# Performance work log

Measured on AMD Instinct MI355X. Metric: run time of the kernel, lower is better.

The kernel has to match this reference:

```python
import jax, jax.numpy as jnp
import numpy as np

NUM_NODES = 100000
NUM_EDGES = 1600000
FEAT = 128
HID = 128
NUM_GRAPHS = 512


def setup_inputs() -> dict:
    key = jax.random.key(0)
    ks = jax.random.split(key, 8)
    x = jax.random.normal(ks[0], (NUM_NODES, FEAT), dtype=jnp.float32)
    edge_index = jax.random.randint(ks[1], (2, NUM_EDGES), 0, NUM_NODES, dtype=jnp.int64)
    batch = jnp.sort(jax.random.randint(ks[2], (NUM_NODES,), 0, NUM_GRAPHS, dtype=jnp.int64))
    # Glorot-ish init for weights (scale named for clarity)
    s1 = 1.0 / np.sqrt(FEAT)
    s2 = 1.0 / np.sqrt(HID)
    W1 = jax.random.normal(ks[3], (FEAT, HID), dtype=jnp.float32) * s1
    b1 = jnp.zeros((HID,), dtype=jnp.float32)
    W2 = jax.random.normal(ks[4], (HID, HID), dtype=jnp.float32) * s2
    b2 = jnp.zeros((HID,), dtype=jnp.float32)
    Wout = jax.random.normal(ks[5], (HID, 1), dtype=jnp.float32) * s2
    bout = jnp.zeros((1,), dtype=jnp.float32)
    return {"x": x, "edge_index": edge_index, "batch": batch,
            "W1": W1, "b1": b1, "W2": W2, "b2": b2, "Wout": Wout, "bout": bout}


def reference(x, edge_index, batch, W1, b1, W2, b2, Wout, bout):
    N = x.shape[0]
    # PyG GCNConv: add self-loops, symmetric normalization D^-1/2 (A+I) D^-1/2
    loops = jnp.arange(N, dtype=edge_index.dtype)
    src = jnp.concatenate([edge_index[0], loops])  # [E+N]
    dst = jnp.concatenate([edge_index[1], loops])  # [E+N]
    ones = jnp.ones_like(dst, dtype=x.dtype)
    deg = jax.ops.segment_sum(ones, dst, num_segments=N)  # in-degree incl. self-loop
    dinv = jnp.where(deg > 0, jax.lax.rsqrt(deg), 0.0)
    coeff = (dinv[src] * dinv[dst])[:, None]  # [E+N, 1]

    def gcn(h, W, b):
        h = h @ W                                       # [N, H] dense GEMM
        msg = h[src] * coeff                            # gather + scale
        agg = jax.ops.segment_sum(msg, dst, num_segments=N)  # scatter-add
        return agg + b

    h = jax.nn.relu(gcn(x, W1, b1))
    h = jax.nn.relu(gcn(h, W2, b2))

    # global_mean_pool over batch ids
    G = NUM_GRAPHS
    sums = jax.ops.segment_sum(h, batch, num_segments=G)
    cnts = jax.ops.segment_sum(jnp.ones((N,), dtype=h.dtype), batch, num_segments=G)
    pooled = sums / jnp.maximum(cnts, 1.0)[:, None]

    return pooled @ Wout + bout  # [G, 1]
```

## Files before the change

### kernel.cpp

```cpp
#include <hip/hip_runtime.h>
#include <hip/hip_bf16.h>
#include <hip/hip_fp16.h>

#define FEAT 128
#define PSLOTS 64
#define BCAP 5120
#define NBIN 512

typedef _Float16 h8 __attribute__((ext_vector_type(8)));
typedef float f4 __attribute__((ext_vector_type(4)));
typedef float fx2 __attribute__((ext_vector_type(2)));


__device__ __forceinline__ void wt_body(const float* __restrict__ W1,
                                        const float* __restrict__ W2,
                                        __half* __restrict__ Wt1,
                                        __half* __restrict__ Wt2, int bid) {
    int t = bid * 256 + threadIdx.x;
    const float* W = (t < 8192) ? W1 : W2;
    __half* Wt     = (t < 8192) ? Wt1 : Wt2;
    int u = t & 8191;
    int n = u >> 6, k2 = (u & 63) * 2;
    float a = W[(size_t)k2 * 128 + n];
    float b = W[(size_t)(k2 + 1) * 128 + n];
    ((__half2*)Wt)[n * 64 + (k2 >> 1)] = __floats2half2_rn(a, b);
}

__device__ __forceinline__ void bin_body(const int* __restrict__ ei, int E, int chunk,
                                         int* __restrict__ cursor,
                                         unsigned* __restrict__ binned, int nb,
                                         int bid, int* smem) {
    int* hist = smem;
    int* base = smem + 512;
    int start = bid * chunk;
    int end = start + chunk; if (end > E) end = E;
    for (int i = threadIdx.x; i < nb; i += 256) hist[i] = 0;
    __syncthreads();
    for (int e = start + threadIdx.x; e < end; e += 256)
        atomicAdd(&hist[ei[E + e] >> 8], 1);
    __syncthreads();
    for (int i = threadIdx.x; i < nb; i += 256) {
        int h = hist[i];
        base[i] = h ? atomicAdd(&cursor[i], h) : 0;
    }
    __syncthreads();
    for (int e = start + threadIdx.x; e < end; e += 256) {
        int s = ei[e];
        int d = ei[E + e];
        int b = d >> 8;
        int pos = atomicAdd(&base[b], 1);
        if (pos < BCAP)
            binned[(size_t)b * BCAP + pos] = (unsigned)s | ((unsigned)(d & 255) << 17);
    }
}

__global__ __launch_bounds__(256) void bin_wt(const int* __restrict__ ei, int E, int chunk,
                                              int* __restrict__ cursor,
                                              unsigned* __restrict__ binned, int nb,
                                              const float* __restrict__ W1,
                                              const float* __restrict__ W2,
                                              __half* __restrict__ Wt1,
                                              __half* __restrict__ Wt2) {
    __shared__ int smem[1024];
    if ((int)blockIdx.x < NBIN)
        bin_body(ei, E, chunk, cursor, binned, nb, blockIdx.x, smem);
    else
        wt_body(W1, W2, Wt1, Wt2, blockIdx.x - NBIN);
}


__device__ __forceinline__ void loadA(const __half* p, int quad, h8* a) {
#pragma unroll
    for (int ks = 0; ks < 4; ++ks)
        a[ks] = *(const h8*)(p + ks * 32 + quad * 8);
}
__device__ __forceinline__ void loadA(const float* p, int quad, h8* a) {
#pragma unroll
    for (int ks = 0; ks < 4; ++ks) {
        const float* q = p + ks * 32 + quad * 8;
        float4 f0 = *(const float4*)q;
        float4 f1 = *(const float4*)(q + 4);
        h8 v;
        v[0] = (_Float16)f0.x; v[1] = (_Float16)f0.y;
        v[2] = (_Float16)f0.z; v[3] = (_Float16)f0.w;
        v[4] = (_Float16)f1.x; v[5] = (_Float16)f1.y;
        v[6] = (_Float16)f1.z; v[7] = (_Float16)f1.w;
        a[ks] = v;
    }
}

template <typename TIN>
__device__ __forceinline__ void gemm_body(const TIN* __restrict__ X,
                                          const __half* __restrict__ Wt,
                                          unsigned char* __restrict__ Y, int N,
                                          const int* __restrict__ deg,
                                          int bid, _Float16* Bs) {
    {
        const float4* src = (const float4*)Wt;
        float4* dst = (float4*)Bs;
        for (int i = threadIdx.x; i < 2048; i += 256) {
            int n = i >> 4, ch = i & 15;
            dst[n * 16 + (ch ^ (n & 15))] = src[i];
        }
    }
    __syncthreads();

    int lane = threadIdx.x & 63;
    int wave = threadIdx.x >> 6;
    int m = lane & 15;
    int quad = lane >> 4;
    int rowb = bid * 128 + wave * 16;

    h8 a[2][4];
#pragma unroll
    for (int rt = 0; rt < 2; ++rt) {
        int rA = rowb + rt * 64 + m; if (rA >= N) rA = N - 1;
        loadA(X + (size_t)rA * FEAT, quad, a[rt]);
    }

    f4 acc[2][8];
#pragma unroll
    for (int rt = 0; rt < 2; ++rt)
#pragma unroll
        for (int nt = 0; nt < 8; ++nt) acc[rt][nt] = (f4){0.f, 0.f, 0.f, 0.f};

#pragma unroll
    for (int nt = 0; nt < 8; ++nt) {
        const _Float16* bbase = Bs + (nt * 16 + m) * 128;
#pragma unroll
        for (int ks = 0; ks < 4; ++ks) {
            int ch = (ks * 4 + quad) ^ m;
            h8 bfrag = *(const h8*)(bbase + ch * 8);
            acc[0][nt] = __builtin_amdgcn_mfma_f32_16x16x32_f16(a[0][ks], bfrag, acc[0][nt], 0, 0, 0);
            acc[1][nt] = __builtin_amdgcn_mfma_f32_16x16x32_f16(a[1][ks], bfrag, acc[1][nt], 0, 0, 0);
        }
    }

#pragma unroll
    for (int rt = 0; rt < 2; ++rt)
#pragma unroll
    for (int r = 0; r < 4; ++r) {
        int row = rowb + rt * 64 + quad * 4 + r;
        if (row < N) {
            float sc = rsqrtf((float)deg[row] + 1.0f);
#pragma unroll
            for (int nt = 0; nt < 8; ++nt) {
                float v = sc * acc[rt][nt][r];
                int pk = __builtin_amdgcn_cvt_pk_fp8_f32(v, v, 0, false);
                Y[(size_t)row * FEAT + nt * 16 + m] = (unsigned char)(pk & 0xFF);
            }
        }
    }
}

template <typename TIN>
__global__ __launch_bounds__(256) void gemm_mfma(const TIN* __restrict__ X,
                                                 const __half* __restrict__ Wt,
                                                 unsigned char* __restrict__ Y,
                                                 const int* __restrict__ deg, int N) {
    __shared__ __align__(16) _Float16 Bs[128 * 128];
    gemm_body<TIN>(X, Wt, Y, N, deg, blockIdx.x, Bs);
}


__global__ __launch_bounds__(256) void k_deg_fill(const unsigned* __restrict__ binned,
                                                  const int* __restrict__ cursor,
                                                  int N, int* __restrict__ deg,
                                                  int* __restrict__ rowstart,
                                                  int* __restrict__ meta, int zoff) {
    __shared__ int ld[256];
    __shared__ int sc[256];
    __shared__ int cur[256];
    int b = blockIdx.x;
    int cnt = cursor[b]; if (cnt > BCAP) cnt = BCAP;
    int s = b * BCAP, e = s + cnt;
    ld[threadIdx.x] = 0;
    __syncthreads();
    for (int i = s + threadIdx.x; i < e; i += 256)
        atomicAdd(&ld[binned[i] >> 17], 1);
    __syncthreads();
    int d = ld[threadIdx.x];
    sc[threadIdx.x] = d;
    __syncthreads();
    for (int off = 1; off < 256; off <<= 1) {
        int t = (threadIdx.x >= off) ? sc[threadIdx.x - off] : 0;
        __syncthreads();
        sc[threadIdx.x] += t;
        __syncthreads();
    }
    int rs = s + sc[threadIdx.x] - d;
    cur[threadIdx.x] = rs;
    int v = (b << 8) + threadIdx.x;
    if (v < N) {
        deg[v] = d;
        rowstart[v] = rs;
    }
    __syncthreads();
    for (int i = s + threadIdx.x; i < e; i += 256) {
        unsigned p = binned[i];
        int src = (int)(p & 0x1FFFF);
        int drl = (int)(p >> 17);
        int pos = atomicAdd(&cur[drl], 1);
        meta[pos] = src << 7;
    }
    int t = cnt + threadIdx.x;
    if (threadIdx.x < 64 && t < BCAP + 64) meta[s + t] = zoff;
}


__device__ __forceinline__ void accum8(uint2 u, fx2* acc) {
    acc[0] += __builtin_amdgcn_cvt_pk_f32_fp8((int)u.x, false);
    acc[1] += __builtin_amdgcn_cvt_pk_f32_fp8((int)u.x, true);
    acc[2] += __builtin_amdgcn_cvt_pk_f32_fp8((int)u.y, false);
    acc[3] += __builtin_amdgcn_cvt_pk_f32_fp8((int)u.y, true);
}

template <bool POOL>
__global__ __launch_bounds__(256) void agg_relu(const unsigned char* __restrict__ Y,
                                                const int* __restrict__ rowstart,
                                                const int* __restrict__ degc,
                                                const int* __restrict__ meta,
                                                const float* __restrict__ bias,
                                                __half* __restrict__ H, int N, int zoff,
                                                const float* __restrict__ Wout,
                                                const int* __restrict__ batch,
                                                float* __restrict__ gsum, int G) {
    int wid  = (blockIdx.x * 256 + threadIdx.x) >> 6;
    int lane = threadIdx.x & 63;
    if (wid >= N) return;
    int v = wid;
    int g = lane >> 4;
    int c = lane & 15;
    int cb = c * 8;
    const char* Ycb = (const char*)Y + cb;

    fx2 acc[4];
#pragma unroll
    for (int k = 0; k < 4; ++k) acc[k] = (fx2){0.f, 0.f};

    {
        int so = (g == 0) ? (v << 7) : zoff;
        uint2 u = *(const uint2*)(Ycb + so);
        accum8(u, acc);
    }

    int base = rowstart[v];
    int n = degc[v];
    int g4 = g * 4;
    for (int i0 = 0; i0 < n; i0 += 16) {
        int o[4];
#pragma unroll
        for (int j = 0; j < 4; ++j) {
            int idx = i0 + g4 + j;
            int mj = meta[base + idx];
            o[j] = (idx < n) ? mj : zoff;
        }
        uint2 u[4];
#pragma unroll
        for (int j = 0; j < 4; ++j)
            u[j] = *(const uint2*)(Ycb + o[j]);
#pragma unroll
        for (int j = 0; j < 4; ++j) accum8(u[j], acc);
    }

#pragma unroll
    for (int k = 0; k < 4; ++k) {
        fx2 t;
        t[0] = __shfl_xor(acc[k][0], 16);
        t[1] = __shfl_xor(acc[k][1], 16);
        acc[k] += t;
        t[0] = __shfl_xor(acc[k][0], 32);
        t[1] = __shfl_xor(acc[k][1], 32);
        acc[k] += t;
    }
    float dv = rsqrtf((float)n + 1.0f);

    if (POOL) {
        const float4* bp = (const float4*)(bias + cb);
        float4 b0 = bp[0], b1 = bp[1];
        const float4* wp = (const float4*)(Wout + cb);
        float4 w0 = wp[0], w1 = wp[1];
        float h0 = fmaxf(dv * acc[0][0] + b0.x, 0.f);
        float h1 = fmaxf(dv * acc[0][1] + b0.y, 0.f);
        float h2 = fmaxf(dv * acc[1][0] + b0.z, 0.f);
        float h3 = fmaxf(dv * acc[1][1] + b0.w, 0.f);
        float h4 = fmaxf(dv * acc[2][0] + b1.x, 0.f);
        float h5 = fmaxf(dv * acc[2][1] + b1.y, 0.f);
        float h6 = fmaxf(dv * acc[3][0] + b1.z, 0.f);
        float h7 = fmaxf(dv * acc[3][1] + b1.w, 0.f);
        float s = h0 * w0.x + h1 * w0.y + h2 * w0.z + h3 * w0.w
                + h4 * w1.x + h5 * w1.y + h6 * w1.z + h7 * w1.w;
        if (g == 0) {
            s += __shfl_xor(s, 1);
            s += __shfl_xor(s, 2);
            s += __shfl_xor(s, 4);
            s += __shfl_xor(s, 8);
            if (lane == 0) {
                int slot = blockIdx.x & (PSLOTS - 1);
                atomicAdd(&gsum[slot * G + batch[v]], s);
            }
        }
    } else {
        fx2 av;
        if (g == 0)      av = acc[0];
        else if (g == 1) av = acc[1];
        else if (g == 2) av = acc[2];
        else             av = acc[3];
        float2 bb = *(const float2*)(bias + cb + g * 2);
        float hx = fmaxf(dv * av[0] + bb.x, 0.f);
        float hy = fmaxf(dv * av[1] + bb.y, 0.f);
        *(__half2*)(H + (size_t)v * FEAT + cb + g * 2) = __floats2half2_rn(hx, hy);
    }
}


__global__ __launch_bounds__(256) void k_head(const float* __restrict__ gsum,
                                              const int* __restrict__ batch, int N, int G,
                                              const float* __restrict__ bout,
                                              float* __restrict__ out) {
    int g = blockIdx.x * 256 + threadIdx.x;
    if (g >= G) return;
    float s = 0.f;
#pragma unroll 8
    for (int k = 0; k < PSLOTS; ++k) s += gsum[k * G + g];
    int lo = 0, hi = N;
    while (lo < hi) { int mid = (lo + hi) >> 1; if (batch[mid] < g) lo = mid + 1; else hi = mid; }
    int start = lo;
    lo = start; hi = N;
    while (lo < hi) { int mid = (lo + hi) >> 1; if (batch[mid] < g + 1) lo = mid + 1; else hi = mid; }
    int cnt = lo - start;
    out[g] = s / (float)(cnt > 0 ? cnt : 1) + bout[0];
}


extern "C" void kernel_launch(void* const* d_in, const int* in_sizes, int n_in,
                              void* d_out, int out_size, void* d_ws, size_t ws_size,
                              hipStream_t stream) {
    const float* x    = (const float*)d_in[0];
    const int*   ei   = (const int*)d_in[1];
    const int*   batch= (const int*)d_in[2];
    const float* W1   = (const float*)d_in[3];
    const float* b1   = (const float*)d_in[4];
    const float* W2   = (const float*)d_in[5];
    const float* b2   = (const float*)d_in[6];
    const float* Wout = (const float*)d_in[7];
    const float* bout = (const float*)d_in[8];

    int N = in_sizes[0] / FEAT;
    int E = in_sizes[1] / 2;
    int G = out_size;
    int nb = (N + 255) >> 8;

    char* ws = (char*)d_ws;
    size_t off = 0;
    auto alloc = [&](size_t bytes) -> void* {
        void* p = ws + off;
        off += (bytes + 255) & ~(size_t)255;
        return p;
    };
    unsigned char* bufY = (unsigned char*)alloc((size_t)N * FEAT);
    __half* bufH     = (__half*)alloc((size_t)N * FEAT * 2);
    __half* Wt1      = (__half*)alloc((size_t)FEAT * FEAT * 2);
    __half* Wt2      = (__half*)alloc((size_t)FEAT * FEAT * 2);
    size_t zbytes    = 256 + (size_t)PSLOTS * G * 4 + (size_t)nb * 4 + (size_t)N * 4;
    char*  zr        = (char*)alloc(zbytes);
    unsigned char* padrow = (unsigned char*)zr;
    float* gsum      = (float*)(zr + 256);
    int*   cursor    = (int*)(gsum + (size_t)PSLOTS * G);
    int*   deg       = cursor + nb;
    int    zoff      = (int)((char*)padrow - (char*)bufY);
    int*   rowstart  = (int*)alloc((size_t)N * 4);
    unsigned* binned = (unsigned*)alloc((size_t)nb * BCAP * 4);
    int*   meta      = (int*)alloc(((size_t)nb * BCAP + 64) * 4);

    int gemm_grid = (N + 127) / 128;
    int agg_grid  = (N + 3) / 4;
    int chunkB = (E + NBIN - 1) / NBIN;

    hipMemsetAsync(zr, 0, zbytes, stream);
    bin_wt<<<NBIN + 64, 256, 0, stream>>>(ei, E, chunkB, cursor, binned, nb,
                                          W1, W2, Wt1, Wt2);
    k_deg_fill<<<nb, 256, 0, stream>>>(binned, cursor, N, deg, rowstart, meta, zoff);
    gemm_mfma<float><<<gemm_grid, 256, 0, stream>>>(x, Wt1, bufY, deg, N);
    agg_relu<false><<<agg_grid, 256, 0, stream>>>(bufY, rowstart, deg, meta, b1, bufH, N, zoff,
                                                  nullptr, nullptr, nullptr, 0);
    gemm_mfma<__half><<<gemm_grid, 256, 0, stream>>>(bufH, Wt2, bufY, deg, N);
    agg_relu<true><<<agg_grid, 256, 0, stream>>>(bufY, rowstart, deg, meta, b2, nullptr, N, zoff,
                                                 Wout, batch, gsum, G);
    k_head<<<(G + 255) / 256, 256, 0, stream>>>(gsum, batch, N, G, bout, (float*)d_out);
}
```

Before: 282.2 us.

## Fuse first GEMM with edge binning and widen aggregation gathers to 16 bytes

Result: slower. 303.3 us (+7.5%).

```diff
diff --git a/kernel.cpp b/kernel.cpp
--- a/kernel.cpp
+++ b/kernel.cpp
@@ -26,6 +26,18 @@
     ((__half2*)Wt)[n * 64 + (k2 >> 1)] = __floats2half2_rn(a, b);
 }
 
+
+__global__ __launch_bounds__(256) void k_init(const float* __restrict__ W1,
+                                              const float* __restrict__ W2,
+                                              __half* __restrict__ Wt1,
+                                              __half* __restrict__ Wt2,
+                                              uint4* __restrict__ zr, int zwords) {
+    if ((int)blockIdx.x < 64) { wt_body(W1, W2, Wt1, Wt2, blockIdx.x); return; }
+    int t = (blockIdx.x - 64) * 256 + threadIdx.x;
+    int stride = (gridDim.x - 64) * 256;
+    for (int i = t; i < zwords; i += stride) zr[i] = make_uint4(0, 0, 0, 0);
+}
+
 __device__ __forceinline__ void bin_body(const int* __restrict__ ei, int E, int chunk,
                                          int* __restrict__ cursor,
                                          unsigned* __restrict__ binned, int nb,
@@ -52,20 +64,6 @@
         if (pos < BCAP)
             binned[(size_t)b * BCAP + pos] = (unsigned)s | ((unsigned)(d & 255) << 17);
     }
-}
-
-__global__ __launch_bounds__(256) void bin_wt(const int* __restrict__ ei, int E, int chunk,
-                                              int* __restrict__ cursor,
-                                              unsigned* __restrict__ binned, int nb,
-                                              const float* __restrict__ W1,
-                                              const float* __restrict__ W2,
-                                              __half* __restrict__ Wt1,
-                                              __half* __restrict__ Wt2) {
-    __shared__ int smem[1024];
-    if ((int)blockIdx.x < NBIN)
-        bin_body(ei, E, chunk, cursor, binned, nb, blockIdx.x, smem);
-    else
-        wt_body(W1, W2, Wt1, Wt2, blockIdx.x - NBIN);
 }
 
 
@@ -89,10 +87,11 @@
     }
 }
 
-template <typename TIN>
+template <typename TIN, bool FP8OUT>
 __device__ __forceinline__ void gemm_body(const TIN* __restrict__ X,
                                           const __half* __restrict__ Wt,
-                                          unsigned char* __restrict__ Y, int N,
+                                          unsigned char* __restrict__ Y,
+                                          __half* __restrict__ Hout, int N,
                                           const int* __restrict__ deg,
                                           int bid, _Float16* Bs) {
     {
@@ -142,24 +141,64 @@
     for (int r = 0; r < 4; ++r) {
         int row = rowb + rt * 64 + quad * 4 + r;
         if (row < N) {
-            float sc = rsqrtf((float)deg[row] + 1.0f);
-#pragma unroll
-            for (int nt = 0; nt < 8; ++nt) {
-                float v = sc * acc[rt][nt][r];
-                int pk = __builtin_amdgcn_cvt_pk_fp8_f32(v, v, 0, false);
-                Y[(size_t)row * FEAT + nt * 16 + m] = (unsigned char)(pk & 0xFF);
+            if (FP8OUT) {
+                float sc = rsqrtf((float)deg[row] + 1.0f);
+#pragma unroll
+                for (int nt = 0; nt < 8; ++nt) {
+                    float v = sc * acc[rt][nt][r];
+                    int pk = __builtin_amdgcn_cvt_pk_fp8_f32(v, v, 0, false);
+                    Y[(size_t)row * FEAT + nt * 16 + m] = (unsigned char)(pk & 0xFF);
+                }
+            } else {
+#pragma unroll
+                for (int nt = 0; nt < 8; ++nt)
+                    Hout[(size_t)row * FEAT + nt * 16 + m] = __float2half(acc[rt][nt][r]);
             }
         }
     }
 }
 
-template <typename TIN>
-__global__ __launch_bounds__(256) void gemm_mfma(const TIN* __restrict__ X,
+
+__global__ __launch_bounds__(256) void gemm_bin(const float* __restrict__ X,
+                                                const __half* __restrict__ Wt1,
+                                                __half* __restrict__ H1, int N, int gemm_grid,
+                                                const int* __restrict__ ei, int E, int chunk,
+                                                int* __restrict__ cursor,
+                                                unsigned* __restrict__ binned, int nb) {
+    __shared__ __align__(16) char smem[32768];
+    if ((int)blockIdx.x < gemm_grid)
+        gemm_body<float, false>(X, Wt1, nullptr, H1, N, nullptr, blockIdx.x, (_Float16*)smem);
+    else
+        bin_body(ei, E, chunk, cursor, binned, nb, blockIdx.x - gemm_grid, (int*)smem);
+}
+
+
+__global__ __launch_bounds__(256) void gemm_mfma(const __half* __restrict__ X,
                                                  const __half* __restrict__ Wt,
                                                  unsigned char* __restrict__ Y,
                                                  const int* __restrict__ deg, int N) {
     __shared__ __align__(16) _Float16 Bs[128 * 128];
-    gemm_body<TIN>(X, Wt, Y, N, deg, blockIdx.x, Bs);
+    gemm_body<__half, true>(X, Wt, Y, nullptr, N, deg, blockIdx.x, Bs);
+}
+
+
+__global__ __launch_bounds__(256) void k_scale(const __half* __restrict__ H1,
+                                               const int* __restrict__ deg,
+                                               unsigned char* __restrict__ Y, int N) {
+    int t = blockIdx.x * 256 + threadIdx.x;
+    if (t >= N * 16) return;
+    int row = t >> 4, c = t & 15;
+    float dv = rsqrtf((float)deg[row] + 1.0f);
+    h8 hv = *(const h8*)(H1 + (size_t)row * FEAT + c * 8);
+    float f0 = dv * (float)hv[0], f1 = dv * (float)hv[1];
+    float f2 = dv * (float)hv[2], f3 = dv * (float)hv[3];
+    float f4_ = dv * (float)hv[4], f5 = dv * (float)hv[5];
+    float f6 = dv * (float)hv[6], f7 = dv * (float)hv[7];
+    int d0 = __builtin_amdgcn_cvt_pk_fp8_f32(f0, f1, 0, false);
+    d0 = __builtin_amdgcn_cvt_pk_fp8_f32(f2, f3, d0, true);
+    int d1 = __builtin_amdgcn_cvt_pk_fp8_f32(f4_, f5, 0, false);
+    d1 = __builtin_amdgcn_cvt_pk_fp8_f32(f6, f7, d1, true);
+    *(uint2*)(Y + (size_t)row * FEAT + c * 8) = make_uint2((unsigned)d0, (unsigned)d1);
 }
 
 
@@ -167,7 +206,7 @@
                                                   const int* __restrict__ cursor,
                                                   int N, int* __restrict__ deg,
                                                   int* __restrict__ rowstart,
-                                                  int* __restrict__ meta, int zoff) {
+                                                  int* __restrict__ meta) {
     __shared__ int ld[256];
     __shared__ int sc[256];
     __shared__ int cur[256];
@@ -203,16 +242,18 @@
         int pos = atomicAdd(&cur[drl], 1);
         meta[pos] = src << 7;
     }
-    int t = cnt + threadIdx.x;
-    if (threadIdx.x < 64 && t < BCAP + 64) meta[s + t] = zoff;
-}
-
-
-__device__ __forceinline__ void accum8(uint2 u, fx2* acc) {
+}
+
+
+__device__ __forceinline__ void accum16(uint4 u, fx2* acc) {
     acc[0] += __builtin_amdgcn_cvt_pk_f32_fp8((int)u.x, false);
     acc[1] += __builtin_amdgcn_cvt_pk_f32_fp8((int)u.x, true);
     acc[2] += __builtin_amdgcn_cvt_pk_f32_fp8((int)u.y, false);
     acc[3] += __builtin_amdgcn_cvt_pk_f32_fp8((int)u.y, true);
+    acc[4] += __builtin_amdgcn_cvt_pk_f32_fp8((int)u.z, false);
+    acc[5] += __builtin_amdgcn_cvt_pk_f32_fp8((int)u.z, true);
+    acc[6] += __builtin_amdgcn_cvt_pk_f32_fp8((int)u.w, false);
+    acc[7] += __builtin_amdgcn_cvt_pk_f32_fp8((int)u.w, true);
 }
 
 template <bool POOL>
@@ -229,43 +270,42 @@
     int lane = threadIdx.x & 63;
     if (wid >= N) return;
     int v = wid;
-    int g = lane >> 4;
-    int c = lane & 15;
-    int cb = c * 8;
+    int g = lane >> 3;
+    int c = lane & 7;
+    int cb = c * 16;
     const char* Ycb = (const char*)Y + cb;
 
-    fx2 acc[4];
-#pragma unroll
-    for (int k = 0; k < 4; ++k) acc[k] = (fx2){0.f, 0.f};
+    fx2 acc[8];
+#pragma unroll
+    for (int k = 0; k < 8; ++k) acc[k] = (fx2){0.f, 0.f};
 
     {
         int so = (g == 0) ? (v << 7) : zoff;
-        uint2 u = *(const uint2*)(Ycb + so);
-        accum8(u, acc);
+        uint4 u = *(const uint4*)(Ycb + so);
+        accum16(u, acc);
     }
 
     int base = rowstart[v];
     int n = degc[v];
-    int g4 = g * 4;
+    int g2 = g * 2;
     for (int i0 = 0; i0 < n; i0 += 16) {
-        int o[4];
-#pragma unroll
-        for (int j = 0; j < 4; ++j) {
-            int idx = i0 + g4 + j;
-            int mj = meta[base + idx];
-            o[j] = (idx < n) ? mj : zoff;
-        }
-        uint2 u[4];
-#pragma unroll
-        for (int j = 0; j < 4; ++j)
-            u[j] = *(const uint2*)(Ycb + o[j]);
-#pragma unroll
-        for (int j = 0; j < 4; ++j) accum8(u[j], acc);
-    }
-
-#pragma unroll
-    for (int k = 0; k < 4; ++k) {
+        int idx0 = i0 + g2, idx1 = idx0 + 1;
+        int m0 = meta[base + idx0];
+        int m1 = meta[base + idx1];
+        int o0 = (idx0 < n) ? m0 : zoff;
+        int o1 = (idx1 < n) ? m1 : zoff;
+        uint4 u0 = *(const uint4*)(Ycb + o0);
+        uint4 u1 = *(const uint4*)(Ycb + o1);
+        accum16(u0, acc);
+        accum16(u1, acc);
+    }
+
+#pragma unroll
+    for (int k = 0; k < 8; ++k) {
         fx2 t;
+        t[0] = __shfl_xor(acc[k][0], 8);
+        t[1] = __shfl_xor(acc[k][1], 8);
+        acc[k] += t;
         t[0] = __shfl_xor(acc[k][0], 16);
         t[1] = __shfl_xor(acc[k][1], 16);
         acc[k] += t;
@@ -277,39 +317,37 @@
 
     if (POOL) {
         const float4* bp = (const float4*)(bias + cb);
-        float4 b0 = bp[0], b1 = bp[1];
         const float4* wp = (const float4*)(Wout + cb);
-        float4 w0 = wp[0], w1 = wp[1];
-        float h0 = fmaxf(dv * acc[0][0] + b0.x, 0.f);
-        float h1 = fmaxf(dv * acc[0][1] + b0.y, 0.f);
-        float h2 = fmaxf(dv * acc[1][0] + b0.z, 0.f);
-        float h3 = fmaxf(dv * acc[1][1] + b0.w, 0.f);
-        float h4 = fmaxf(dv * acc[2][0] + b1.x, 0.f);
-        float h5 = fmaxf(dv * acc[2][1] + b1.y, 0.f);
-        float h6 = fmaxf(dv * acc[3][0] + b1.z, 0.f);
-        float h7 = fmaxf(dv * acc[3][1] + b1.w, 0.f);
-        float s = h0 * w0.x + h1 * w0.y + h2 * w0.z + h3 * w0.w
-                + h4 * w1.x + h5 * w1.y + h6 * w1.z + h7 * w1.w;
-        if (g == 0) {
-            s += __shfl_xor(s, 1);
-            s += __shfl_xor(s, 2);
-            s += __shfl_xor(s, 4);
-            s += __shfl_xor(s, 8);
-            if (lane == 0) {
-                int slot = blockIdx.x & (PSLOTS - 1);
-                atomicAdd(&gsum[slot * G + batch[v]], s);
-            }
+        float s = 0.f;
+#pragma unroll
+        for (int k = 0; k < 4; ++k) {
+            float4 b4 = bp[k], w4 = wp[k];
+            s += fmaxf(dv * acc[2 * k][0] + b4.x, 0.f) * w4.x;
+            s += fmaxf(dv * acc[2 * k][1] + b4.y, 0.f) * w4.y;
+            s += fmaxf(dv * acc[2 * k + 1][0] + b4.z, 0.f) * w4.z;
+            s += fmaxf(dv * acc[2 * k + 1][1] + b4.w, 0.f) * w4.w;
+        }
+        s += __shfl_xor(s, 1);
+        s += __shfl_xor(s, 2);
+        s += __shfl_xor(s, 4);
+        if (lane == 0) {
+            int slot = blockIdx.x & (PSLOTS - 1);
+            atomicAdd(&gsum[slot * G + batch[v]], s);
         }
     } else {
         fx2 av;
         if (g == 0)      av = acc[0];
         else if (g == 1) av = acc[1];
         else if (g == 2) av = acc[2];
-        else             av = acc[3];
-        float2 bb = *(const float2*)(bias + cb + g * 2);
+        else if (g == 3) av = acc[3];
+        else if (g == 4) av = acc[4];
+        else if (g == 5) av = acc[5];
+        else if (g == 6) av = acc[6];
+        else             av = acc[7];
+        float2 bb = *(const float2*)(bias + cb + g2);
         float hx = fmaxf(dv * av[0] + bb.x, 0.f);
         float hy = fmaxf(dv * av[1] + bb.y, 0.f);
-        *(__half2*)(H + (size_t)v * FEAT + cb + g * 2) = __floats2half2_rn(hx, hy);
+        *(__half2*)(H + (size_t)v * FEAT + cb + g2) = __floats2half2_rn(hx, hy);
     }
 }
 
@@ -376,15 +414,16 @@
     int gemm_grid = (N + 127) / 128;
     int agg_grid  = (N + 3) / 4;
     int chunkB = (E + NBIN - 1) / NBIN;
-
-    hipMemsetAsync(zr, 0, zbytes, stream);
-    bin_wt<<<NBIN + 64, 256, 0, stream>>>(ei, E, chunkB, cursor, binned, nb,
-                                          W1, W2, Wt1, Wt2);
-    k_deg_fill<<<nb, 256, 0, stream>>>(binned, cursor, N, deg, rowstart, meta, zoff);
-    gemm_mfma<float><<<gemm_grid, 256, 0, stream>>>(x, Wt1, bufY, deg, N);
+    int zwords = (int)((zbytes + 15) / 16);
+
+    k_init<<<224, 256, 0, stream>>>(W1, W2, Wt1, Wt2, (uint4*)zr, zwords);
+    gemm_bin<<<gemm_grid + NBIN, 256, 0, stream>>>(x, Wt1, bufH, N, gemm_grid,
+                                                   ei, E, chunkB, cursor, binned, nb);
+    k_deg_fill<<<nb, 256, 0, stream>>>(binned, cursor, N, deg, rowstart, meta);
+    k_scale<<<(N * 16 + 255) / 256, 256, 0, stream>>>(bufH, deg, bufY, N);
     agg_relu<false><<<agg_grid, 256, 0, stream>>>(bufY, rowstart, deg, meta, b1, bufH, N, zoff,
                                                   nullptr, nullptr, nullptr, 0);
-    gemm_mfma<__half><<<gemm_grid, 256, 0, stream>>>(bufH, Wt2, bufY, deg, N);
+    gemm_mfma<<<gemm_grid, 256, 0, stream>>>(bufH, Wt2, bufY, deg, N);
     agg_relu<true><<<agg_grid, 256, 0, stream>>>(bufY, rowstart, deg, meta, b2, nullptr, N, zoff,
                                                  Wout, batch, gsum, G);
     k_head<<<(G + 255) / 256, 256, 0, stream>>>(gsum, batch, N, G, bout, (float*)d_out);
```

## Overlap first-layer GEMM with edge binning and defer degree scaling to fill kernel

Applied to the files above, without the earlier changes.

New measurement: 282.5 us. No clear change (+0.1%).

```diff
diff --git a/kernel.cpp b/kernel.cpp
--- a/kernel.cpp
+++ b/kernel.cpp
@@ -26,6 +26,18 @@
     ((__half2*)Wt)[n * 64 + (k2 >> 1)] = __floats2half2_rn(a, b);
 }
 
+
+__global__ __launch_bounds__(256) void k_init(const float* __restrict__ W1,
+                                              const float* __restrict__ W2,
+                                              __half* __restrict__ Wt1,
+                                              __half* __restrict__ Wt2,
+                                              uint4* __restrict__ zr, int zwords) {
+    if ((int)blockIdx.x < 64) { wt_body(W1, W2, Wt1, Wt2, blockIdx.x); return; }
+    int t = (blockIdx.x - 64) * 256 + threadIdx.x;
+    int stride = (gridDim.x - 64) * 256;
+    for (int i = t; i < zwords; i += stride) zr[i] = make_uint4(0, 0, 0, 0);
+}
+
 __device__ __forceinline__ void bin_body(const int* __restrict__ ei, int E, int chunk,
                                          int* __restrict__ cursor,
                                          unsigned* __restrict__ binned, int nb,
@@ -52,20 +64,6 @@
         if (pos < BCAP)
             binned[(size_t)b * BCAP + pos] = (unsigned)s | ((unsigned)(d & 255) << 17);
     }
-}
-
-__global__ __launch_bounds__(256) void bin_wt(const int* __restrict__ ei, int E, int chunk,
-                                              int* __restrict__ cursor,
-                                              unsigned* __restrict__ binned, int nb,
-                                              const float* __restrict__ W1,
-                                              const float* __restrict__ W2,
-                                              __half* __restrict__ Wt1,
-                                              __half* __restrict__ Wt2) {
-    __shared__ int smem[1024];
-    if ((int)blockIdx.x < NBIN)
-        bin_body(ei, E, chunk, cursor, binned, nb, blockIdx.x, smem);
-    else
-        wt_body(W1, W2, Wt1, Wt2, blockIdx.x - NBIN);
 }
 
 
@@ -89,10 +87,11 @@
     }
 }
 
-template <typename TIN>
+template <typename TIN, bool FP8OUT>
 __device__ __forceinline__ void gemm_body(const TIN* __restrict__ X,
                                           const __half* __restrict__ Wt,
-                                          unsigned char* __restrict__ Y, int N,
+                                          unsigned char* __restrict__ Y,
+                                          __half* __restrict__ Hout, int N,
                                           const int* __restrict__ deg,
                                           int bid, _Float16* Bs) {
     {
@@ -142,24 +141,44 @@
     for (int r = 0; r < 4; ++r) {
         int row = rowb + rt * 64 + quad * 4 + r;
         if (row < N) {
-            float sc = rsqrtf((float)deg[row] + 1.0f);
-#pragma unroll
-            for (int nt = 0; nt < 8; ++nt) {
-                float v = sc * acc[rt][nt][r];
-                int pk = __builtin_amdgcn_cvt_pk_fp8_f32(v, v, 0, false);
-                Y[(size_t)row * FEAT + nt * 16 + m] = (unsigned char)(pk & 0xFF);
+            if (FP8OUT) {
+                float sc = rsqrtf((float)deg[row] + 1.0f);
+#pragma unroll
+                for (int nt = 0; nt < 8; ++nt) {
+                    float v = sc * acc[rt][nt][r];
+                    int pk = __builtin_amdgcn_cvt_pk_fp8_f32(v, v, 0, false);
+                    Y[(size_t)row * FEAT + nt * 16 + m] = (unsigned char)(pk & 0xFF);
+                }
+            } else {
+#pragma unroll
+                for (int nt = 0; nt < 8; ++nt)
+                    Hout[(size_t)row * FEAT + nt * 16 + m] = __float2half(acc[rt][nt][r]);
             }
         }
     }
 }
 
-template <typename TIN>
-__global__ __launch_bounds__(256) void gemm_mfma(const TIN* __restrict__ X,
+
+__global__ __launch_bounds__(256) void gemm_bin(const float* __restrict__ X,
+                                                const __half* __restrict__ Wt1,
+                                                __half* __restrict__ H1, int N, int gemm_grid,
+                                                const int* __restrict__ ei, int E, int chunk,
+                                                int* __restrict__ cursor,
+                                                unsigned* __restrict__ binned, int nb) {
+    __shared__ __align__(16) char smem[32768];
+    if ((int)blockIdx.x < gemm_grid)
+        gemm_body<float, false>(X, Wt1, nullptr, H1, N, nullptr, blockIdx.x, (_Float16*)smem);
+    else
+        bin_body(ei, E, chunk, cursor, binned, nb, blockIdx.x - gemm_grid, (int*)smem);
+}
+
+
+__global__ __launch_bounds__(256) void gemm_mfma(const __half* __restrict__ X,
                                                  const __half* __restrict__ Wt,
                                                  unsigned char* __restrict__ Y,
                                                  const int* __restrict__ deg, int N) {
     __shared__ __align__(16) _Float16 Bs[128 * 128];
-    gemm_body<TIN>(X, Wt, Y, N, deg, blockIdx.x, Bs);
+    gemm_body<__half, true>(X, Wt, Y, nullptr, N, deg, blockIdx.x, Bs);
 }
 
 
@@ -167,7 +186,9 @@
                                                   const int* __restrict__ cursor,
                                                   int N, int* __restrict__ deg,
                                                   int* __restrict__ rowstart,
-                                                  int* __restrict__ meta, int zoff) {
+                                                  int* __restrict__ meta,
+                                                  const __half* __restrict__ H1,
+                                                  unsigned char* __restrict__ Y) {
     __shared__ int ld[256];
     __shared__ int sc[256];
     __shared__ int cur[256];
@@ -203,8 +224,26 @@
         int pos = atomicAdd(&cur[drl], 1);
         meta[pos] = src << 7;
     }
-    int t = cnt + threadIdx.x;
-    if (threadIdx.x < 64 && t < BCAP + 64) meta[s + t] = zoff;
+    int rowb = b << 8;
+#pragma unroll
+    for (int it = 0; it < 16; ++it) {
+        int idx = it * 256 + threadIdx.x;
+        int rr = idx >> 4, c = idx & 15;
+        int row = rowb + rr;
+        if (row < N) {
+            float dv = rsqrtf((float)ld[rr] + 1.0f);
+            h8 hv = *(const h8*)(H1 + (size_t)row * FEAT + c * 8);
+            float f0 = dv * (float)hv[0], f1 = dv * (float)hv[1];
+            float f2 = dv * (float)hv[2], f3 = dv * (float)hv[3];
+            float f4_ = dv * (float)hv[4], f5 = dv * (float)hv[5];
+            float f6 = dv * (float)hv[6], f7 = dv * (float)hv[7];
+            int d0 = __builtin_amdgcn_cvt_pk_fp8_f32(f0, f1, 0, false);
+            d0 = __builtin_amdgcn_cvt_pk_fp8_f32(f2, f3, d0, true);
+            int d1 = __builtin_amdgcn_cvt_pk_fp8_f32(f4_, f5, 0, false);
+            d1 = __builtin_amdgcn_cvt_pk_fp8_f32(f6, f7, d1, true);
+            *(uint2*)(Y + (size_t)row * FEAT + c * 8) = make_uint2((unsigned)d0, (unsigned)d1);
+        }
+    }
 }
 
 
@@ -376,15 +415,15 @@
     int gemm_grid = (N + 127) / 128;
     int agg_grid  = (N + 3) / 4;
     int chunkB = (E + NBIN - 1) / NBIN;
-
-    hipMemsetAsync(zr, 0, zbytes, stream);
-    bin_wt<<<NBIN + 64, 256, 0, stream>>>(ei, E, chunkB, cursor, binned, nb,
-                                          W1, W2, Wt1, Wt2);
-    k_deg_fill<<<nb, 256, 0, stream>>>(binned, cursor, N, deg, rowstart, meta, zoff);
-    gemm_mfma<float><<<gemm_grid, 256, 0, stream>>>(x, Wt1, bufY, deg, N);
+    int zwords = (int)((zbytes + 15) / 16);
+
+    k_init<<<224, 256, 0, stream>>>(W1, W2, Wt1, Wt2, (uint4*)zr, zwords);
+    gemm_bin<<<gemm_grid + NBIN, 256, 0, stream>>>(x, Wt1, bufH, N, gemm_grid,
+                                                   ei, E, chunkB, cursor, binned, nb);
+    k_deg_fill<<<nb, 256, 0, stream>>>(binned, cursor, N, deg, rowstart, meta, bufH, bufY);
     agg_relu<false><<<agg_grid, 256, 0, stream>>>(bufY, rowstart, deg, meta, b1, bufH, N, zoff,
                                                   nullptr, nullptr, nullptr, 0);
-    gemm_mfma<__half><<<gemm_grid, 256, 0, stream>>>(bufH, Wt2, bufY, deg, N);
+    gemm_mfma<<<gemm_grid, 256, 0, stream>>>(bufH, Wt2, bufY, deg, N);
     agg_relu<true><<<agg_grid, 256, 0, stream>>>(bufY, rowstart, deg, meta, b2, nullptr, N, zoff,
                                                  Wout, batch, gsum, G);
     k_head<<<(G + 255) / 256, 256, 0, stream>>>(gsum, batch, N, G, bout, (float*)d_out);
```
